# Performance work log

Measured on AMD Instinct MI355X. Metric: run time of the kernel, lower is better.

The kernel has to match this reference:

```python
import jax, jax.numpy as jnp
import numpy as np

BATCH = 4096
TEMP = 0.5
WORLD = 1
B = BATCH * WORLD
N = 2 * B
DIM = 128


def _neg_indices():
    # mask_correlated_samples: ones(N,N) with diagonal and the two +/-B
    # off-diagonals zeroed; negatives are entries where mask is True.
    mask = np.ones((N, N), dtype=bool)
    np.fill_diagonal(mask, False)
    idx = np.arange(B)
    mask[idx, idx + B] = False
    mask[idx + B, idx] = False
    rows, cols = np.nonzero(mask)  # each row has exactly N-2 negatives
    return rows.reshape(N, N - 2), cols.reshape(N, N - 2)

_NEG_ROWS, _NEG_COLS = _neg_indices()


def setup_inputs() -> dict:
    key = jax.random.key(0)
    k1, k2 = jax.random.split(key)
    z_i = jax.random.normal(k1, (BATCH, DIM), dtype=jnp.float32)
    z_j = jax.random.normal(k2, (BATCH, DIM), dtype=jnp.float32)
    return {"z_i": z_i, "z_j": z_j}


def reference(z_i, z_j):
    z = jnp.concatenate([z_i, z_j], axis=0)                 # [N, D]
    z = z / jnp.linalg.norm(z, axis=1, keepdims=True)       # L2 normalize
    # cosine similarity of unit vectors == dot product
    sim = (z @ z.T) / TEMP                                   # [N, N]
    sim_i_j = jnp.diagonal(sim, offset=B)                    # [B]
    sim_j_i = jnp.diagonal(sim, offset=-B)                   # [B]
    pos = jnp.concatenate([sim_i_j, sim_j_i])[:, None]       # [N, 1]
    neg = sim[_NEG_ROWS, _NEG_COLS]                          # [N, N-2]
    logits = jnp.concatenate([pos, neg], axis=1)             # [N, N-1]
    # CrossEntropyLoss(reduction='sum') with labels all zero, then / N
    loss = jnp.sum(jax.scipy.special.logsumexp(logits, axis=1) - logits[:, 0])
    return loss / N
```

## Files before the change

### kernel.cpp

```cpp
#include <hip/hip_runtime.h>
#include <hip/hip_bf16.h>


#define NN 8192
#define BHALF 4096
#define DIMK 128

typedef __bf16 bf16x8 __attribute__((ext_vector_type(8)));
typedef float f32x4 __attribute__((ext_vector_type(4)));

#define C1F 2.8853900817779268f
#define SCALEF 1.6986436f

__global__ __launch_bounds__(256) void nt_normalize(
    const float* __restrict__ zi, const float* __restrict__ zj,
    unsigned int* __restrict__ zb_packed, float* __restrict__ out) {
  if (blockIdx.x == 0 && threadIdx.x == 0) out[0] = 0.0f;
  int row = blockIdx.x * 4 + (threadIdx.x >> 6);
  int lane = threadIdx.x & 63;
  const float* src = (row < BHALF) ? (zi + (size_t)row * DIMK)
                                   : (zj + (size_t)(row - BHALF) * DIMK);
  float2 v = ((const float2*)src)[lane];
  float ss = v.x * v.x + v.y * v.y;
#pragma unroll
  for (int off = 32; off >= 1; off >>= 1) ss += __shfl_xor(ss, off, 64);
  float rn = rsqrtf(ss) * SCALEF;
  __hip_bfloat16 h0 = __float2bfloat16(v.x * rn);
  __hip_bfloat16 h1 = __float2bfloat16(v.y * rn);
  unsigned int packed = ((unsigned int)(*(unsigned short*)&h1) << 16) |
                        (*(unsigned short*)&h0);
  int tile = row >> 4, t = row & 15;
  int cq = lane >> 2;
  int c = cq >> 2, quad = cq & 3;
  size_t widx = ((size_t)((tile * 4 + c) * 64 + quad * 16 + t)) * 4 + (lane & 3);
  zb_packed[widx] = packed;
}

__global__ __launch_bounds__(256, 2) void nt_sim(
    const uint4* __restrict__ zbv, float* __restrict__ part) {
  __shared__ uint4 ldsb[4096];

  const int lane = threadIdx.x & 63;
  const int wave = threadIdx.x >> 6;
  const int quad = lane >> 4;
  const int t = lane & 15;
  const int row_tile0 = blockIdx.y * 16 + wave * 4;

  {
    const char* gsrc = (const char*)zbv + (size_t)blockIdx.x * 65536;
#pragma unroll
    for (int k = 0; k < 16; ++k) {
      int chunk = k * 4 + wave;
      __builtin_amdgcn_global_load_lds(
          (const __attribute__((address_space(1))) unsigned int*)(
              gsrc + chunk * 1024 + lane * 16),
          (__attribute__((address_space(3))) unsigned int*)(
              (char*)ldsb + chunk * 1024),
          16, 0, 0);
    }
  }

  bf16x8 A[4][4];
#pragma unroll
  for (int rt = 0; rt < 4; ++rt)
#pragma unroll
    for (int c = 0; c < 4; ++c)
      A[rt][c] = __builtin_bit_cast(
          bf16x8, zbv[(size_t)((row_tile0 + rt) * 4 + c) * 64 + lane]);

  float sum[4][4];
#pragma unroll
  for (int rt = 0; rt < 4; ++rt)
#pragma unroll
    for (int r = 0; r < 4; ++r) sum[rt][r] = 0.f;

  __syncthreads();

#pragma unroll 2
  for (int ct = 0; ct < 16; ++ct) {
    f32x4 acc[4];
#pragma unroll
    for (int rt = 0; rt < 4; ++rt) acc[rt] = (f32x4){0.f, 0.f, 0.f, 0.f};
#pragma unroll
    for (int c = 0; c < 4; ++c) {
      bf16x8 bv = __builtin_bit_cast(bf16x8, ldsb[(ct * 4 + c) * 64 + lane]);
#pragma unroll
      for (int rt = 0; rt < 4; ++rt)
        acc[rt] = __builtin_amdgcn_mfma_f32_16x16x32_bf16(A[rt][c], bv,
                                                          acc[rt], 0, 0, 0);
    }
#pragma unroll
    for (int rt = 0; rt < 4; ++rt)
#pragma unroll
      for (int r = 0; r < 4; ++r)
        sum[rt][r] += __builtin_amdgcn_exp2f(acc[rt][r]);
  }

#pragma unroll
  for (int off = 8; off >= 1; off >>= 1)
#pragma unroll
    for (int rt = 0; rt < 4; ++rt)
#pragma unroll
      for (int r = 0; r < 4; ++r)
        sum[rt][r] += __shfl_xor(sum[rt][r], off, 16);

  if (t == 0) {
    float* dst = part + (size_t)blockIdx.x * NN;
    int row_base = row_tile0 * 16;
#pragma unroll
    for (int rt = 0; rt < 4; ++rt)
#pragma unroll
      for (int r = 0; r < 4; ++r)
        dst[row_base + rt * 16 + quad * 4 + r] = sum[rt][r];
  }
}

__device__ __forceinline__ float bf2f(unsigned short s) {
  unsigned int u = (unsigned int)s << 16;
  return __builtin_bit_cast(float, u);
}

__global__ __launch_bounds__(256) void nt_finalize(
    const uint4* __restrict__ zbv, const float* __restrict__ part,
    float* __restrict__ out) {
  int i = blockIdx.x * 256 + threadIdx.x;
  int tile = i >> 4, t = i & 15;
  int p = i ^ BHALF;
  int tilep = p >> 4;
  float S = 0.f;
#pragma unroll
  for (int k = 0; k < 32; ++k) S += part[(size_t)k * NN + i];
  float dp = 0.f, dd = 0.f;
#pragma unroll
  for (int cq = 0; cq < 16; ++cq) {
    int c = cq >> 2, q = cq & 3;
    uint4 ua = zbv[(size_t)((tile * 4 + c) * 64 + q * 16 + t)];
    uint4 up = zbv[(size_t)((tilep * 4 + c) * 64 + q * 16 + t)];
    const unsigned short* pa = (const unsigned short*)&ua;
    const unsigned short* pp = (const unsigned short*)&up;
#pragma unroll
    for (int k = 0; k < 8; ++k) {
      float a = bf2f(pa[k]), pv = bf2f(pp[k]);
      dd = fmaf(a, a, dd);
      dp = fmaf(a, pv, dp);
    }
  }
  float diag = __builtin_amdgcn_exp2f(dd);
  float v = logf(S - diag) - (2.0f / C1F) * dp;
#pragma unroll
  for (int off = 32; off >= 1; off >>= 1) v += __shfl_xor(v, off, 64);
  __shared__ float wsum[4];
  if ((threadIdx.x & 63) == 0) wsum[threadIdx.x >> 6] = v;
  __syncthreads();
  if (threadIdx.x == 0)
    atomicAdd(out, (wsum[0] + wsum[1] + wsum[2] + wsum[3]) * (1.0f / (float)NN));
}

extern "C" void kernel_launch(void* const* d_in, const int* in_sizes, int n_in,
                              void* d_out, int out_size, void* d_ws,
                              size_t ws_size, hipStream_t stream) {
  const float* zi = (const float*)d_in[0];
  const float* zj = (const float*)d_in[1];

  unsigned int* zb = (unsigned int*)d_ws;
  float* part = (float*)((char*)d_ws + (2u << 20));

  nt_normalize<<<NN / 4, 256, 0, stream>>>(zi, zj, zb, (float*)d_out);

  dim3 grid(32, 32);
  nt_sim<<<grid, 256, 0, stream>>>((const uint4*)zb, part);

  nt_finalize<<<NN / 256, 256, 0, stream>>>((const uint4*)zb, part,
                                            (float*)d_out);
}
```

Baseline: 80.82 us.

## Exploit symmetry of similarity matrix by computing only upper-triangular block pairs

```diff
diff --git a/kernel.cpp b/kernel.cpp
--- a/kernel.cpp
+++ b/kernel.cpp
@@ -37,17 +37,25 @@
 }
 
 __global__ __launch_bounds__(256, 2) void nt_sim(
-    const uint4* __restrict__ zbv, float* __restrict__ part) {
+    const uint4* __restrict__ zbv, float* __restrict__ partR,
+    float* __restrict__ partC) {
   __shared__ uint4 ldsb[4096];
+  __shared__ float colbuf[4][256];
+
+  const int bid = blockIdx.x;
+  int p = (int)((65.0f - sqrtf(4225.0f - 8.0f * (float)bid)) * 0.5f);
+  while (p > 0 && p * (65 - p) / 2 > bid) --p;
+  while ((p + 1) * (64 - p) / 2 <= bid) ++p;
+  const int q = p + (bid - p * (65 - p) / 2);
 
   const int lane = threadIdx.x & 63;
   const int wave = threadIdx.x >> 6;
   const int quad = lane >> 4;
   const int t = lane & 15;
-  const int row_tile0 = blockIdx.y * 16 + wave * 4;
+  const int row_tile0 = p * 16 + wave * 4;
 
   {
-    const char* gsrc = (const char*)zbv + (size_t)blockIdx.x * 65536;
+    const char* gsrc = (const char*)zbv + (size_t)q * 65536;
 #pragma unroll
     for (int k = 0; k < 16; ++k) {
       int chunk = k * 4 + wave;
@@ -73,6 +81,7 @@
   for (int rt = 0; rt < 4; ++rt)
 #pragma unroll
     for (int r = 0; r < 4; ++r) sum[rt][r] = 0.f;
+  float colw[16];
 
   __syncthreads();
 
@@ -89,11 +98,16 @@
         acc[rt] = __builtin_amdgcn_mfma_f32_16x16x32_bf16(A[rt][c], bv,
                                                           acc[rt], 0, 0, 0);
     }
+    float cp = 0.f;
 #pragma unroll
     for (int rt = 0; rt < 4; ++rt)
 #pragma unroll
-      for (int r = 0; r < 4; ++r)
-        sum[rt][r] += __builtin_amdgcn_exp2f(acc[rt][r]);
+      for (int r = 0; r < 4; ++r) {
+        float e = __builtin_amdgcn_exp2f(acc[rt][r]);
+        sum[rt][r] += e;
+        cp += e;
+      }
+    colw[ct] = cp;
   }
 
 #pragma unroll
@@ -105,13 +119,29 @@
         sum[rt][r] += __shfl_xor(sum[rt][r], off, 16);
 
   if (t == 0) {
-    float* dst = part + (size_t)blockIdx.x * NN;
-    int row_base = row_tile0 * 16;
+    float* dst = partR + (size_t)q * NN + p * 256 + wave * 64;
 #pragma unroll
     for (int rt = 0; rt < 4; ++rt)
 #pragma unroll
       for (int r = 0; r < 4; ++r)
-        dst[row_base + rt * 16 + quad * 4 + r] = sum[rt][r];
+        dst[rt * 16 + quad * 4 + r] = sum[rt][r];
+  }
+
+  if (p != q) {
+#pragma unroll
+    for (int ct = 0; ct < 16; ++ct) {
+      colw[ct] += __shfl_xor(colw[ct], 16, 64);
+      colw[ct] += __shfl_xor(colw[ct], 32, 64);
+    }
+    if (quad == 0) {
+#pragma unroll
+      for (int ct = 0; ct < 16; ++ct) colbuf[wave][ct * 16 + t] = colw[ct];
+    }
+    __syncthreads();
+    int cidx = threadIdx.x;
+    float tot = colbuf[0][cidx] + colbuf[1][cidx] + colbuf[2][cidx] +
+                colbuf[3][cidx];
+    partC[(size_t)p * NN + q * 256 + cidx] = tot;
   }
 }
 
@@ -121,21 +151,22 @@
 }
 
 __global__ __launch_bounds__(256) void nt_finalize(
-    const uint4* __restrict__ zbv, const float* __restrict__ part,
-    float* __restrict__ out) {
+    const uint4* __restrict__ zbv, const float* __restrict__ partR,
+    const float* __restrict__ partC, float* __restrict__ out) {
   int i = blockIdx.x * 256 + threadIdx.x;
+  int s = blockIdx.x;
   int tile = i >> 4, t = i & 15;
-  int p = i ^ BHALF;
-  int tilep = p >> 4;
+  int pr = i ^ BHALF;
+  int tilep = pr >> 4;
   float S = 0.f;
-#pragma unroll
-  for (int k = 0; k < 32; ++k) S += part[(size_t)k * NN + i];
+  for (int k = s; k < 32; ++k) S += partR[(size_t)k * NN + i];
+  for (int k = 0; k < s; ++k) S += partC[(size_t)k * NN + i];
   float dp = 0.f, dd = 0.f;
 #pragma unroll
   for (int cq = 0; cq < 16; ++cq) {
-    int c = cq >> 2, q = cq & 3;
-    uint4 ua = zbv[(size_t)((tile * 4 + c) * 64 + q * 16 + t)];
-    uint4 up = zbv[(size_t)((tilep * 4 + c) * 64 + q * 16 + t)];
+    int c = cq >> 2, qq = cq & 3;
+    uint4 ua = zbv[(size_t)((tile * 4 + c) * 64 + qq * 16 + t)];
+    uint4 up = zbv[(size_t)((tilep * 4 + c) * 64 + qq * 16 + t)];
     const unsigned short* pa = (const unsigned short*)&ua;
     const unsigned short* pp = (const unsigned short*)&up;
 #pragma unroll
@@ -163,13 +194,13 @@
   const float* zj = (const float*)d_in[1];
 
   unsigned int* zb = (unsigned int*)d_ws;
-  float* part = (float*)((char*)d_ws + (2u << 20));
+  float* partR = (float*)((char*)d_ws + (2u << 20));
+  float* partC = (float*)((char*)d_ws + (3u << 20));
 
   nt_normalize<<<NN / 4, 256, 0, stream>>>(zi, zj, zb, (float*)d_out);
 
-  dim3 grid(32, 32);
-  nt_sim<<<grid, 256, 0, stream>>>((const uint4*)zb, part);
-
-  nt_finalize<<<NN / 256, 256, 0, stream>>>((const uint4*)zb, part,
+  nt_sim<<<528, 256, 0, stream>>>((const uint4*)zb, partR, partC);
+
+  nt_finalize<<<NN / 256, 256, 0, stream>>>((const uint4*)zb, partR, partC,
                                             (float*)d_out);
 }
```

After: 90.84 us. 1.12x slower.
